# Optimization experiments

Hardware: AMD Instinct MI355X
Metric: run time of the kernel (lower is better)

Reference implementation:

```python
import jax, jax.numpy as jnp
import numpy as np

N = 1_000_000          # number of RoIs
C = 4                  # num_class (foreground classes)
IMG_H, IMG_W = 1080.0, 1920.0
BBOX_MEAN = jnp.array([0.0, 0.0, 0.0, 0.0], jnp.float32)
BBOX_STD = jnp.array([0.1, 0.1, 0.2, 0.2], jnp.float32)
THR_OBJ = 0.2          # threshold_objectness
THR_CLS = 0.1          # thresholds[0]
MIN_W, MIN_H = 6.0, 6.0
MAX_CAND = 300         # nms max_candidate_n
OVERLAP = 0.5          # nms overlap_ratio
TOP_N = 100            # nms top_n


def setup_inputs() -> dict:
    key = jax.random.key(0)
    k1, k2, k3, k4, k5 = jax.random.split(key, 5)
    logits = jax.random.normal(k1, (N, C + 1), jnp.float32) * 2.0
    cls_score_softmax = jax.nn.softmax(logits, axis=-1)          # rows sum to 1, like softmax output
    bbox_pred = jax.random.normal(k2, (N, 4 * (C + 1)), jnp.float32) * 0.5
    x1 = jax.random.uniform(k3, (N,), jnp.float32, 0.0, IMG_W * 0.8)
    y1 = jax.random.uniform(k4, (N,), jnp.float32, 0.0, IMG_H * 0.8)
    wh = jax.random.uniform(k5, (N, 2), jnp.float32, 8.0, 200.0)
    rois = jnp.stack([jnp.zeros((N,), jnp.float32), x1, y1, x1 + wh[:, 0], y1 + wh[:, 1]], axis=1)
    im_info = jnp.array([IMG_H, IMG_W], jnp.float32)
    return {"cls_score_softmax": cls_score_softmax, "bbox_pred": bbox_pred, "rois": rois, "im_info": im_info}


def _pairwise_iou(b):
    # torchvision box_iou convention: area = (x2-x1)*(y2-y1), no +1
    lt = jnp.maximum(b[:, None, :2], b[None, :, :2])
    rb = jnp.minimum(b[:, None, 2:], b[None, :, 2:])
    wh = jnp.clip(rb - lt, 0.0)
    inter = wh[..., 0] * wh[..., 1]
    area = (b[:, 2] - b[:, 0]) * (b[:, 3] - b[:, 1])
    return inter / (area[:, None] + area[None, :] - inter)


def _forward(cls_score_softmax, bbox_pred, rois, im_info):
    h_img, w_img = im_info[0], im_info[1]
    # denormalize deltas and decode against rois (bbox_transform_inv_rcnn)
    deltas = (bbox_pred.reshape(-1, 4) * BBOX_STD + BBOX_MEAN).reshape(-1, C + 1, 4)
    bx = rois[:, 1:]
    w = bx[:, 2] - bx[:, 0] + 1.0
    h = bx[:, 3] - bx[:, 1] + 1.0
    cx = bx[:, 0] + 0.5 * (w - 1.0)
    cy = bx[:, 1] + 0.5 * (h - 1.0)
    pcx = deltas[:, :, 0] * w[:, None] + cx[:, None]
    pcy = deltas[:, :, 1] * h[:, None] + cy[:, None]
    pw = jnp.exp(deltas[:, :, 2]) * w[:, None]
    ph = jnp.exp(deltas[:, :, 3]) * h[:, None]
    pred = jnp.stack([pcx - 0.5 * (pw - 1.0), pcy - 0.5 * (ph - 1.0),
                      pcx + 0.5 * (pw - 1.0), pcy + 0.5 * (ph - 1.0)], axis=-1)  # [N, C+1, 4]
    # refine_out_of_map_bbox: clip to image
    pred = jnp.stack([jnp.clip(pred[..., 0], 0.0, w_img - 1.0),
                      jnp.clip(pred[..., 1], 0.0, h_img - 1.0),
                      jnp.clip(pred[..., 2], 0.0, w_img - 1.0),
                      jnp.clip(pred[..., 3], 0.0, h_img - 1.0)], axis=-1)
    # objectness + class-score filters (masked instead of compacted: jit-friendly)
    mask_obj = (1.0 - cls_score_softmax[:, 0]) >= THR_OBJ
    maxes = jnp.max(cls_score_softmax[:, 1:], axis=1)
    argmaxes = jnp.argmax(cls_score_softmax[:, 1:], axis=1) + 1
    mask_cls = maxes > THR_CLS
    # select the box of the argmax class per row
    box = jnp.take_along_axis(pred, argmaxes[:, None, None], axis=1)[:, 0, :]  # [N, 4]
    bw = box[:, 2] - box[:, 0] + 1.0
    bh = box[:, 3] - box[:, 1] + 1.0
    mask_size = (bw >= MIN_W) | (bh >= MIN_H)  # HEIGHT_OR_WIDTH
    valid = mask_obj & mask_cls & mask_size
    # top-k candidates by max class prob (invalid rows pushed below any real score)
    cand_scores = jnp.where(valid, maxes, -1.0)
    top_vals, top_idx = jax.lax.top_k(cand_scores, MAX_CAND)   # sorted descending
    cand_boxes = box[top_idx]                                   # [M, 4]
    cand_probs = cls_score_softmax[top_idx]                     # [M, C+1]
    cand_valid = top_vals > -0.5
    # greedy NMS over the (score-sorted) candidates
    iou = _pairwise_iou(cand_boxes)
    idx = jnp.arange(MAX_CAND)

    def body(i, keep):
        sup = keep[i] & (iou[i] > OVERLAP) & (idx > i)
        return keep & ~sup

    keep = jax.lax.fori_loop(0, MAX_CAND, body, cand_valid)
    # compact kept rows into the first TOP_N slots (drop-row scatter trick)
    order = jnp.cumsum(keep.astype(jnp.int32)) - 1
    slot = jnp.where(keep & (order < TOP_N), order, TOP_N)
    rows = jnp.concatenate([jnp.zeros((MAX_CAND, 1), cand_boxes.dtype), cand_boxes, cand_probs], axis=1)
    out = jnp.zeros((TOP_N + 1, rows.shape[1]), rows.dtype).at[slot].set(rows)[:TOP_N]
    return out  # [TOP_N, 1 + 4 + (C+1)] = [100, 10], zero-padded past the kept count


def reference(cls_score_softmax, bbox_pred, rois, im_info):
    return _forward(cls_score_softmax, bbox_pred, rois, im_info)
```

## Files before the change

### kernel.cpp

```cpp
#include <hip/hip_runtime.h>
#include <math.h>

#define NBINS 4096
#define CAP   4096
#define MAXC  300
#define MAXCP 320
#define NTASK (MAXC*5)
#define TOPN  100

__device__ __forceinline__ void decode4(float x1, float y1, float x2, float y2,
                                        float4 d4, float Wimg, float Himg,
                                        float& bx1, float& by1, float& bx2, float& by2)
{
    float w  = x2 - x1 + 1.0f;
    float h  = y2 - y1 + 1.0f;
    float cx = x1 + 0.5f*(w - 1.0f);
    float cy = y1 + 0.5f*(h - 1.0f);
    float d0 = d4.x*0.1f, d1 = d4.y*0.1f, d2 = d4.z*0.2f, d3 = d4.w*0.2f;
    float pcx = d0*w + cx;
    float pcy = d1*h + cy;
    float pw  = expf(d2)*w;
    float ph  = expf(d3)*h;
    bx1 = fminf(fmaxf(pcx - 0.5f*(pw-1.0f), 0.0f), Wimg-1.0f);
    by1 = fminf(fmaxf(pcy - 0.5f*(ph-1.0f), 0.0f), Himg-1.0f);
    bx2 = fminf(fmaxf(pcx + 0.5f*(pw-1.0f), 0.0f), Wimg-1.0f);
    by2 = fminf(fmaxf(pcy + 0.5f*(ph-1.0f), 0.0f), Himg-1.0f);
}

__global__ __launch_bounds__(256)
void rcnn_pass1(const float4* __restrict__ cls4, const float4* __restrict__ bbox4,
                const float4* __restrict__ rois4, const float* __restrict__ iminfo,
                float4* __restrict__ scores4,
                unsigned int* __restrict__ hist, unsigned int* __restrict__ counter, int Ng)
{
    if (blockIdx.x == 0) {
        for (int k = threadIdx.x; k < NBINS; k += 256) hist[k] = 0u;
        if (threadIdx.x == 0) *counter = 0u;
    }

    int g = blockIdx.x * blockDim.x + threadIdx.x;
    if (g >= Ng) return;

    float c[20], q[20];
    #pragma unroll
    for (int v = 0; v < 5; v++) {
        float4 cv = cls4[5*g + v];
        c[4*v] = cv.x; c[4*v+1] = cv.y; c[4*v+2] = cv.z; c[4*v+3] = cv.w;
        float4 rv = rois4[5*g + v];
        q[4*v] = rv.x; q[4*v+1] = rv.y; q[4*v+2] = rv.z; q[4*v+3] = rv.w;
    }
    float Himg = iminfo[0], Wimg = iminfo[1];

    float s[4];
    #pragma unroll
    for (int j = 0; j < 4; j++) {
        float p0 = c[5*j], p1 = c[5*j+1], p2 = c[5*j+2], p3 = c[5*j+3], p4 = c[5*j+4];
        float m = p1; int a = 1;
        if (p2 > m) { m = p2; a = 2; }
        if (p3 > m) { m = p3; a = 3; }
        if (p4 > m) { m = p4; a = 4; }
        float sc = -1.0f;
        if (((1.0f - p0) >= 0.2f) && (m > 0.1f)) {
            float4 d4 = bbox4[20*g + 5*j + a];
            float bx1, by1, bx2, by2;
            decode4(q[5*j+1], q[5*j+2], q[5*j+3], q[5*j+4], d4, Wimg, Himg, bx1, by1, bx2, by2);
            float bw = bx2 - bx1 + 1.0f;
            float bh = by2 - by1 + 1.0f;
            if ((bw >= 6.0f) || (bh >= 6.0f)) sc = m;
        }
        s[j] = sc;
    }
    scores4[g] = make_float4(s[0], s[1], s[2], s[3]);
}

__global__ __launch_bounds__(1024)
void rcnn_hist(const float4* __restrict__ scores4, unsigned int* __restrict__ hist, int Ng)
{
    __shared__ unsigned int lh[NBINS];
    const int t = threadIdx.x;
    for (int k = t; k < NBINS; k += 1024) lh[k] = 0u;
    __syncthreads();

    int stride = gridDim.x * 1024;
    for (int g = blockIdx.x * 1024 + t; g < Ng; g += stride) {
        float4 s4 = scores4[g];
        float ss[4] = { s4.x, s4.y, s4.z, s4.w };
        #pragma unroll
        for (int j = 0; j < 4; j++) {
            float s = ss[j];
            if (s > -0.5f) {
                int bin = (int)(s * (float)NBINS);
                bin = bin > NBINS-1 ? NBINS-1 : bin;
                atomicAdd(&lh[bin], 1u);
            }
        }
    }
    __syncthreads();
    for (int k = t; k < NBINS; k += 1024) {
        unsigned int v = lh[k];
        if (v) atomicAdd(&hist[k], v);
    }
}

__global__ __launch_bounds__(64)
void rcnn_pass2(const unsigned int* __restrict__ hist, int* __restrict__ taubin)
{
    const int t = threadIdx.x;
    const uint4* h4 = (const uint4*)hist;
    uint4 v[16];
    #pragma unroll
    for (int j = 0; j < 16; j++) v[j] = h4[t*16 + j];
    unsigned int chunk = 0;
    #pragma unroll
    for (int j = 0; j < 16; j++) chunk += v[j].x + v[j].y + v[j].z + v[j].w;

    unsigned int sfx = chunk;
    #pragma unroll
    for (int d = 1; d < 64; d <<= 1) {
        unsigned int o = __shfl_down(sfx, d, 64);
        if (t + d < 64) sfx += o;
    }
    unsigned int nxt = sfx - chunk;
    bool found = (sfx >= MAXC) && (nxt < MAXC);
    unsigned long long bal = __ballot(found);
    if (found) {
        unsigned int cum = nxt;
        int tau = 64*t;
        #pragma unroll
        for (int k = 15; k >= 0; k--) {
            cum += v[k].w; if (cum >= MAXC) { tau = 64*t + 4*k + 3; goto done; }
            cum += v[k].z; if (cum >= MAXC) { tau = 64*t + 4*k + 2; goto done; }
            cum += v[k].y; if (cum >= MAXC) { tau = 64*t + 4*k + 1; goto done; }
            cum += v[k].x; if (cum >= MAXC) { tau = 64*t + 4*k + 0; goto done; }
        }
        done:
        *taubin = tau;
    }
    if (bal == 0ull && t == 0) *taubin = 0;
}

__global__ __launch_bounds__(256)
void rcnn_pass3(const float4* __restrict__ scores4, const int* __restrict__ taubin,
                float* __restrict__ cscore, int* __restrict__ cidx,
                unsigned int* __restrict__ counter, int Ng)
{
    int g = blockIdx.x * blockDim.x + threadIdx.x;
    if (g >= Ng) return;
    float4 s4 = scores4[g];
    int tau = *taubin;
    float ss[4] = { s4.x, s4.y, s4.z, s4.w };
    #pragma unroll
    for (int j = 0; j < 4; j++) {
        float s = ss[j];
        if (s > -0.5f) {
            int bin = (int)(s * (float)NBINS);
            bin = bin > NBINS-1 ? NBINS-1 : bin;
            if (bin >= tau) {
                unsigned int pos = atomicAdd(counter, 1u);
                if (pos < CAP) { cscore[pos] = s; cidx[pos] = 4*g + j; }
            }
        }
    }
}

__global__ __launch_bounds__(1024)
void rcnn_rank(const float* __restrict__ cls, const float* __restrict__ bbox,
               const float* __restrict__ rois, const float* __restrict__ iminfo,
               const float* __restrict__ cscore, const int* __restrict__ cidx,
               const unsigned int* __restrict__ counter,
               float4* __restrict__ bxg, float* __restrict__ areag,
               float* __restrict__ prg, unsigned long long* __restrict__ maskg)
{
    __shared__ __align__(16) float s_s[CAP];
    __shared__ __align__(16) int   s_id[CAP];
    __shared__ int tid_[MAXC];
    __shared__ unsigned long long maskw[5];
    const int t  = threadIdx.x;
    const int NT = 1024;
    int M = (int)*counter; if (M > CAP) M = CAP;

    for (int i = t; i < M; i += NT)  { s_s[i] = cscore[i]; s_id[i] = cidx[i]; }
    for (int r = t; r < MAXC; r += NT) tid_[r] = -1;
    if (t < 5) maskw[t] = 0ull;
    __syncthreads();

    {
        const float4* sv = (const float4*)s_s;
        const int4*   dv = (const int4*)s_id;
        int M4 = M >> 2;
        for (int i = t; i < M; i += NT) {
            float si = s_s[i]; int di = s_id[i];
            int r = 0;
            for (int jj = 0; jj < M4; jj++) {
                float4 sj = sv[jj]; int4 dj = dv[jj];
                r += (sj.x > si) || (sj.x == si && dj.x < di);
                r += (sj.y > si) || (sj.y == si && dj.y < di);
                r += (sj.z > si) || (sj.z == si && dj.z < di);
                r += (sj.w > si) || (sj.w == si && dj.w < di);
            }
            for (int j = M4 << 2; j < M; j++) {
                float sj = s_s[j]; int dj = s_id[j];
                r += (sj > si) || (sj == si && dj < di);
            }
            if (r < MAXC) tid_[r] = di;
        }
    }
    __syncthreads();

    float Himg = iminfo[0], Wimg = iminfo[1];
    for (int r = t; r < MAXCP; r += NT) {
        int i = (r < MAXC) ? tid_[r] : -1;
        float4 bx = make_float4(0.0f, 0.0f, 0.0f, 0.0f);
        float ar = 0.0f;
        if (i >= 0) {
            float p0 = cls[5*i], p1 = cls[5*i+1], p2 = cls[5*i+2], p3 = cls[5*i+3], p4 = cls[5*i+4];
            prg[5*r+0]=p0; prg[5*r+1]=p1; prg[5*r+2]=p2; prg[5*r+3]=p3; prg[5*r+4]=p4;
            float m = p1; int a = 1;
            if (p2 > m) { m = p2; a = 2; }
            if (p3 > m) { m = p3; a = 3; }
            if (p4 > m) { m = p4; a = 4; }
            float4 d4 = ((const float4*)bbox)[5*i + a];
            float bx1, by1, bx2, by2;
            decode4(rois[5*i+1], rois[5*i+2], rois[5*i+3], rois[5*i+4], d4, Wimg, Himg, bx1, by1, bx2, by2);
            bx = make_float4(bx1, by1, bx2, by2);
            ar = (bx2-bx1)*(by2-by1);
            atomicOr(&maskw[r>>6], 1ull << (r & 63));
        }
        bxg[r] = bx; areag[r] = ar;
    }
    __syncthreads();
    if (t < 5) maskg[t] = maskw[t];
}

__global__ __launch_bounds__(64)
void rcnn_sup(const float4* __restrict__ bxg, const float* __restrict__ areag,
              const unsigned long long* __restrict__ maskg,
              unsigned long long* __restrict__ supg)
{
    __shared__ float4 bxs[MAXCP];
    __shared__ float  ars[MAXCP];
    const int t = threadIdx.x;
    for (int r = t; r < MAXCP; r += 64) { bxs[r] = bxg[r]; ars[r] = areag[r]; }
    __syncthreads();

    int task = blockIdx.x * 64 + t;
    if (task >= NTASK) return;
    int w = task / MAXC;
    int i = task - w * MAXC;
    unsigned long long bits = 0ull;
    int j0 = w << 6;
    if (j0 + 63 > i) {
        float4 bi = bxs[i];
        float areaA = ars[i];
        for (int b = 0; b < 64; b++) {
            int j = j0 + b;
            float4 bj = bxs[j];
            float lx = fmaxf(bi.x, bj.x), ly = fmaxf(bi.y, bj.y);
            float rx = fminf(bi.z, bj.z), ry = fminf(bi.w, bj.w);
            float iw = fmaxf(rx - lx, 0.0f), ih = fmaxf(ry - ly, 0.0f);
            float inter = iw * ih;
            float iou = inter / (areaA + ars[j] - inter);
            bits |= (iou > 0.5f) ? (1ull << b) : 0ull;
        }
        unsigned long long jgt = (i < j0) ? ~0ull
                              : ((i - j0) >= 63 ? 0ull : ~((1ull << (i - j0 + 1)) - 1ull));
        bits &= jgt & maskg[w];
    }
    supg[i*6 + w] = bits;
}

__global__ __launch_bounds__(1024)
void rcnn_scan(const float4* __restrict__ bxg, const float* __restrict__ prg,
               const unsigned long long* __restrict__ maskg,
               const unsigned long long* __restrict__ supg, float* __restrict__ out)
{
    __shared__ __align__(16) unsigned long long sup[MAXC*6];
    __shared__ unsigned long long maskw[5];
    __shared__ float orows[TOPN*10];
    __shared__ int   kept_list[TOPN];
    __shared__ int   s_kept;
    const int t  = threadIdx.x;
    const int NT = 1024;

    {
        const ulonglong2* sg2 = (const ulonglong2*)supg;
        ulonglong2* sl2 = (ulonglong2*)sup;
        for (int k = t; k < (MAXC*6)/2; k += NT) sl2[k] = sg2[k];
    }
    if (t < 5) maskw[t] = maskg[t];
    for (int k = t; k < TOPN*10; k += NT) orows[k] = 0.0f;
    __syncthreads();

    if (t == 0) {
        unsigned long long k0=maskw[0], k1=maskw[1], k2=maskw[2], k3=maskw[3], k4=maskw[4];
        int kept = 0;
        #define SCAN_WORD(W, KW)                                                   \
        if (kept < TOPN) {                                                         \
            unsigned long long donem = 0ull;                                       \
            for (;;) {                                                             \
                unsigned long long rem = (KW) & ~donem;                            \
                if (!rem) break;                                                   \
                int b = __builtin_ctzll(rem);                                      \
                int i = (W << 6) + b;                                              \
                kept_list[kept++] = i;                                             \
                if (kept >= TOPN) break;                                           \
                unsigned long long s0 = sup[i*6+0], s1 = sup[i*6+1],               \
                                   s2 = sup[i*6+2], s3 = sup[i*6+3],               \
                                   s4 = sup[i*6+4];                                \
                k0 &= ~s0; k1 &= ~s1; k2 &= ~s2; k3 &= ~s3; k4 &= ~s4;             \
                donem = (b == 63) ? ~0ull : ((2ull << b) - 1ull);                  \
            }                                                                      \
        }
        SCAN_WORD(0, k0)
        SCAN_WORD(1, k1)
        SCAN_WORD(2, k2)
        SCAN_WORD(3, k3)
        SCAN_WORD(4, k4)
        #undef SCAN_WORD
        s_kept = kept;
    }
    __syncthreads();

    int kept = s_kept;
    if (t < kept) {
        int r = kept_list[t];
        float4 bx = bxg[r];
        float* row = &orows[t*10];
        row[0] = 0.0f;
        row[1] = bx.x; row[2] = bx.y; row[3] = bx.z; row[4] = bx.w;
        row[5] = prg[5*r+0]; row[6] = prg[5*r+1]; row[7] = prg[5*r+2];
        row[8] = prg[5*r+3]; row[9] = prg[5*r+4];
    }
    __syncthreads();
    for (int k = t; k < TOPN*10; k += NT) out[k] = orows[k];
}

extern "C" void kernel_launch(void* const* d_in, const int* in_sizes, int n_in,
                              void* d_out, int out_size, void* d_ws, size_t ws_size,
                              hipStream_t stream)
{
    const float* cls    = (const float*)d_in[0];
    const float* bbox   = (const float*)d_in[1];
    const float* rois   = (const float*)d_in[2];
    const float* iminfo = (const float*)d_in[3];
    int N  = in_sizes[0] / 5;
    int Ng = N / 4;

    char* ws = (char*)d_ws;
    float* scores = (float*)ws;
    size_t off = ((size_t)N * 4 + 255) & ~(size_t)255;
    unsigned int* hist    = (unsigned int*)(ws + off); off += NBINS * 4;
    int*          taubin  = (int*)(ws + off);          off += 256;
    unsigned int* counter = (unsigned int*)(ws + off); off += 256;
    float*        cscore  = (float*)(ws + off);        off += CAP * 4;
    int*          cidx    = (int*)(ws + off);          off += CAP * 4;
    float4*       bxg     = (float4*)(ws + off);       off += MAXCP * 16;
    float*        areag   = (float*)(ws + off);        off += ((MAXCP * 4 + 255) & ~(size_t)255);
    float*        prg     = (float*)(ws + off);        off += ((MAXC * 5 * 4 + 255) & ~(size_t)255);
    unsigned long long* maskg = (unsigned long long*)(ws + off); off += 256;
    unsigned long long* supg  = (unsigned long long*)(ws + off); off += MAXC * 6 * 8;

    int blocksG = (Ng + 255) / 256;
    rcnn_pass1<<<blocksG, 256, 0, stream>>>((const float4*)cls, (const float4*)bbox,
                                            (const float4*)rois, iminfo,
                                            (float4*)scores, hist, counter, Ng);
    rcnn_hist<<<64, 1024, 0, stream>>>((const float4*)scores, hist, Ng);
    rcnn_pass2<<<1, 64, 0, stream>>>(hist, taubin);
    rcnn_pass3<<<blocksG, 256, 0, stream>>>((const float4*)scores, taubin,
                                            cscore, cidx, counter, Ng);
    rcnn_rank<<<1, 1024, 0, stream>>>(cls, bbox, rois, iminfo,
                                      cscore, cidx, counter,
                                      bxg, areag, prg, maskg);
    rcnn_sup<<<(NTASK + 63) / 64, 64, 0, stream>>>(bxg, areag, maskg, supg);
    rcnn_scan<<<1, 1024, 0, stream>>>(bxg, prg, maskg, supg, (float*)d_out);
}
```

Before: 206.5 us.

## Fuse the RCNN post-processing pipeline into a single cooperative grid-synced kernel

Replaces the seven-kernel chain with one cooperative kernel of 256 blocks x 1024 threads, using grid.sync between phases. The phases are scoring plus histogram, global histogram merge, threshold search, candidate compaction, ranking with decode, the IoU suppression bitmask and the greedy scan. The histogram is built in shared memory right in the scoring pass, and scores stay in registers, so the scores buffer is no longer written and re-read. The O(M^2) rank step is spread across all blocks instead of one block. In exchange it adds five grid-wide barriers and depends on the cooperative launch succeeding; if the launch fails, it falls back to the old multi-kernel path.

```diff
diff --git a/kernel.cpp b/kernel.cpp
--- a/kernel.cpp
+++ b/kernel.cpp
@@ -1,5 +1,8 @@
 #include <hip/hip_runtime.h>
+#include <hip/hip_cooperative_groups.h>
 #include <math.h>
+
+namespace cg = cooperative_groups;
 
 #define NBINS 4096
 #define CAP   4096
@@ -7,6 +10,8 @@
 #define MAXCP 320
 #define NTASK (MAXC*5)
 #define TOPN  100
+#define NBLK  256
+#define NTHR  1024
 
 __device__ __forceinline__ void decode4(float x1, float y1, float x2, float y2,
                                         float4 d4, float Wimg, float Himg,
@@ -27,6 +32,287 @@
     by2 = fminf(fmaxf(pcy + 0.5f*(ph-1.0f), 0.0f), Himg-1.0f);
 }
 
+__global__ __launch_bounds__(NTHR)
+void rcnn_mega(const float* __restrict__ cls, const float* __restrict__ bbox,
+               const float* __restrict__ rois, const float* __restrict__ iminfo,
+               char* __restrict__ ws, float* __restrict__ out, int Ng)
+{
+    size_t off = ((size_t)Ng * 16 + 255) & ~(size_t)255;
+    unsigned int* hist    = (unsigned int*)(ws + off); off += NBINS*4;
+    off += 256;
+    unsigned int* counter = (unsigned int*)(ws + off); off += 256;
+    float*  cscore        = (float*)(ws + off);        off += CAP*4;
+    int*    cidx          = (int*)(ws + off);          off += CAP*4;
+    float4* bxg           = (float4*)(ws + off);       off += MAXCP*16;
+    float*  areag         = (float*)(ws + off);        off += ((MAXCP*4 + 255) & ~(size_t)255);
+    float*  prg           = (float*)(ws + off);        off += ((MAXC*5*4 + 255) & ~(size_t)255);
+    unsigned long long* maskg = (unsigned long long*)(ws + off); off += 256;
+    unsigned long long* supg  = (unsigned long long*)(ws + off);
+
+    __shared__ __align__(16) unsigned char u_smem[32768];
+    __shared__ __align__(16) float4 bxs[MAXCP];
+    __shared__ float ars[MAXCP];
+    __shared__ float orows[TOPN*10];
+    __shared__ int   kept_list[TOPN];
+    __shared__ int   s_misc[2];
+
+    cg::grid_group grid = cg::this_grid();
+    const int t   = threadIdx.x;
+    const int bid = blockIdx.x;
+    const int g   = bid * NTHR + t;
+
+    unsigned int* lh = (unsigned int*)u_smem;
+    for (int k = t; k < NBINS; k += NTHR) lh[k] = 0u;
+    if (bid == 0) {
+        for (int k = t; k < NBINS; k += NTHR) hist[k] = 0u;
+        if (t == 0) *counter = 0u;
+        if (t < 5)  maskg[t] = 0ull;
+        for (int r = t; r < MAXCP; r += NTHR) {
+            bxg[r] = make_float4(0.0f, 0.0f, 0.0f, 0.0f);
+            areag[r] = 0.0f;
+        }
+    }
+    __syncthreads();
+
+    float s[4] = { -1.0f, -1.0f, -1.0f, -1.0f };
+    if (g < Ng) {
+        const float4* cls4  = (const float4*)cls;
+        const float4* rois4 = (const float4*)rois;
+        const float4* bbox4 = (const float4*)bbox;
+        float c[20], q[20];
+        #pragma unroll
+        for (int v = 0; v < 5; v++) {
+            float4 cv = cls4[5*g + v];
+            c[4*v] = cv.x; c[4*v+1] = cv.y; c[4*v+2] = cv.z; c[4*v+3] = cv.w;
+            float4 rv = rois4[5*g + v];
+            q[4*v] = rv.x; q[4*v+1] = rv.y; q[4*v+2] = rv.z; q[4*v+3] = rv.w;
+        }
+        float Himg = iminfo[0], Wimg = iminfo[1];
+        #pragma unroll
+        for (int j = 0; j < 4; j++) {
+            float p0 = c[5*j], p1 = c[5*j+1], p2 = c[5*j+2], p3 = c[5*j+3], p4 = c[5*j+4];
+            float m = p1; int a = 1;
+            if (p2 > m) { m = p2; a = 2; }
+            if (p3 > m) { m = p3; a = 3; }
+            if (p4 > m) { m = p4; a = 4; }
+            float sc = -1.0f;
+            if (((1.0f - p0) >= 0.2f) && (m > 0.1f)) {
+                float4 d4 = bbox4[20*g + 5*j + a];
+                float bx1, by1, bx2, by2;
+                decode4(q[5*j+1], q[5*j+2], q[5*j+3], q[5*j+4], d4, Wimg, Himg, bx1, by1, bx2, by2);
+                float bw = bx2 - bx1 + 1.0f;
+                float bh = by2 - by1 + 1.0f;
+                if ((bw >= 6.0f) || (bh >= 6.0f)) sc = m;
+            }
+            s[j] = sc;
+            if (sc > -0.5f) {
+                int bin = (int)(sc * (float)NBINS);
+                bin = bin > NBINS-1 ? NBINS-1 : bin;
+                atomicAdd(&lh[bin], 1u);
+            }
+        }
+    }
+    __threadfence();
+    grid.sync();
+
+    for (int k = t; k < NBINS; k += NTHR) {
+        unsigned int v = lh[k];
+        if (v) atomicAdd(&hist[k], v);
+    }
+    __threadfence();
+    grid.sync();
+
+    if (t < 64) {
+        const uint4* h4 = (const uint4*)hist;
+        uint4 v[16];
+        #pragma unroll
+        for (int j = 0; j < 16; j++) v[j] = h4[t*16 + j];
+        unsigned int chunk = 0;
+        #pragma unroll
+        for (int j = 0; j < 16; j++) chunk += v[j].x + v[j].y + v[j].z + v[j].w;
+        unsigned int sfx = chunk;
+        #pragma unroll
+        for (int d = 1; d < 64; d <<= 1) {
+            unsigned int o = __shfl_down(sfx, d, 64);
+            if (t + d < 64) sfx += o;
+        }
+        unsigned int nxt = sfx - chunk;
+        bool found = (sfx >= MAXC) && (nxt < MAXC);
+        unsigned long long bal = __ballot(found);
+        if (found) {
+            unsigned int cum = nxt;
+            int tauv = 64*t;
+            #pragma unroll
+            for (int k = 15; k >= 0; k--) {
+                cum += v[k].w; if (cum >= MAXC) { tauv = 64*t + 4*k + 3; goto dtau; }
+                cum += v[k].z; if (cum >= MAXC) { tauv = 64*t + 4*k + 2; goto dtau; }
+                cum += v[k].y; if (cum >= MAXC) { tauv = 64*t + 4*k + 1; goto dtau; }
+                cum += v[k].x; if (cum >= MAXC) { tauv = 64*t + 4*k + 0; goto dtau; }
+            }
+            dtau:
+            s_misc[0] = tauv;
+        }
+        if (bal == 0ull && t == 0) s_misc[0] = 0;
+    }
+    __syncthreads();
+    {
+        int tau = s_misc[0];
+        if (g < Ng) {
+            #pragma unroll
+            for (int j = 0; j < 4; j++) {
+                float sc = s[j];
+                if (sc > -0.5f) {
+                    int bin = (int)(sc * (float)NBINS);
+                    bin = bin > NBINS-1 ? NBINS-1 : bin;
+                    if (bin >= tau) {
+                        unsigned int pos = atomicAdd(counter, 1u);
+                        if (pos < CAP) { cscore[pos] = sc; cidx[pos] = 4*g + j; }
+                    }
+                }
+            }
+        }
+    }
+    __threadfence();
+    grid.sync();
+
+    {
+        float* s_s  = (float*)u_smem;
+        int*   s_id = (int*)(u_smem + CAP*4);
+        int M = (int)*counter; if (M > CAP) M = CAP;
+        for (int i = t; i < M; i += NTHR) { s_s[i] = cscore[i]; s_id[i] = cidx[i]; }
+        __syncthreads();
+
+        int C = (M + NBLK - 1) / NBLK;
+        float Himg = iminfo[0], Wimg = iminfo[1];
+        const float4* sv = (const float4*)s_s;
+        const int4*   dv = (const int4*)s_id;
+        int M4 = M >> 2;
+        for (int ii = t; ii < C; ii += NTHR) {
+            int i = bid * C + ii;
+            if (i < M) {
+                float si = s_s[i]; int di = s_id[i];
+                int r = 0;
+                for (int jj = 0; jj < M4; jj++) {
+                    float4 sj = sv[jj]; int4 dj = dv[jj];
+                    r += (sj.x > si) || (sj.x == si && dj.x < di);
+                    r += (sj.y > si) || (sj.y == si && dj.y < di);
+                    r += (sj.z > si) || (sj.z == si && dj.z < di);
+                    r += (sj.w > si) || (sj.w == si && dj.w < di);
+                }
+                for (int j = M4 << 2; j < M; j++) {
+                    float sj = s_s[j]; int dj = s_id[j];
+                    r += (sj > si) || (sj == si && dj < di);
+                }
+                if (r < MAXC) {
+                    int idx = di;
+                    float p0 = cls[5*idx], p1 = cls[5*idx+1], p2 = cls[5*idx+2],
+                          p3 = cls[5*idx+3], p4 = cls[5*idx+4];
+                    prg[5*r+0]=p0; prg[5*r+1]=p1; prg[5*r+2]=p2; prg[5*r+3]=p3; prg[5*r+4]=p4;
+                    float m = p1; int a = 1;
+                    if (p2 > m) { m = p2; a = 2; }
+                    if (p3 > m) { m = p3; a = 3; }
+                    if (p4 > m) { m = p4; a = 4; }
+                    float4 d4 = ((const float4*)bbox)[5*idx + a];
+                    float bx1, by1, bx2, by2;
+                    decode4(rois[5*idx+1], rois[5*idx+2], rois[5*idx+3], rois[5*idx+4],
+                            d4, Wimg, Himg, bx1, by1, bx2, by2);
+                    bxg[r] = make_float4(bx1, by1, bx2, by2);
+                    areag[r] = (bx2-bx1)*(by2-by1);
+                    atomicOr(&maskg[r>>6], 1ull << (r & 63));
+                }
+            }
+        }
+    }
+    __threadfence();
+    grid.sync();
+
+    {
+        for (int r = t; r < MAXCP; r += NTHR) { bxs[r] = bxg[r]; ars[r] = areag[r]; }
+        __syncthreads();
+        if (t < 6) {
+            int task = bid * 6 + t;
+            if (task < NTASK) {
+                int w = task / MAXC;
+                int i = task - w * MAXC;
+                unsigned long long bits = 0ull;
+                int j0 = w << 6;
+                if (j0 + 63 > i) {
+                    float4 bi = bxs[i];
+                    float areaA = ars[i];
+                    for (int b = 0; b < 64; b++) {
+                        int j = j0 + b;
+                        float4 bj = bxs[j];
+                        float lx = fmaxf(bi.x, bj.x), ly = fmaxf(bi.y, bj.y);
+                        float rx = fminf(bi.z, bj.z), ry = fminf(bi.w, bj.w);
+                        float iw = fmaxf(rx - lx, 0.0f), ih = fmaxf(ry - ly, 0.0f);
+                        float inter = iw * ih;
+                        float iou = inter / (areaA + ars[j] - inter);
+                        bits |= (iou > 0.5f) ? (1ull << b) : 0ull;
+                    }
+                    unsigned long long jgt = (i < j0) ? ~0ull
+                                          : ((i - j0) >= 63 ? 0ull : ~((1ull << (i - j0 + 1)) - 1ull));
+                    bits &= jgt & maskg[w];
+                }
+                supg[i*6 + w] = bits;
+            }
+        }
+    }
+    __threadfence();
+    grid.sync();
+
+    if (bid == 0) {
+        unsigned long long* sup = (unsigned long long*)u_smem;
+        const ulonglong2* sg2 = (const ulonglong2*)supg;
+        ulonglong2* sl2 = (ulonglong2*)sup;
+        for (int k = t; k < (MAXC*6)/2; k += NTHR) sl2[k] = sg2[k];
+        for (int k = t; k < TOPN*10; k += NTHR) orows[k] = 0.0f;
+        __syncthreads();
+
+        if (t == 0) {
+            unsigned long long k0=maskg[0], k1=maskg[1], k2=maskg[2], k3=maskg[3], k4=maskg[4];
+            int kept = 0;
+            #define SCAN_WORD(W, KW)                                                   \
+            if (kept < TOPN) {                                                         \
+                unsigned long long donem = 0ull;                                       \
+                for (;;) {                                                             \
+                    unsigned long long rem = (KW) & ~donem;                            \
+                    if (!rem) break;                                                   \
+                    int b = __builtin_ctzll(rem);                                      \
+                    int i = (W << 6) + b;                                              \
+                    kept_list[kept++] = i;                                             \
+                    if (kept >= TOPN) break;                                           \
+                    unsigned long long s0 = sup[i*6+0], s1 = sup[i*6+1],               \
+                                       s2 = sup[i*6+2], s3 = sup[i*6+3],               \
+                                       s4 = sup[i*6+4];                                \
+                    k0 &= ~s0; k1 &= ~s1; k2 &= ~s2; k3 &= ~s3; k4 &= ~s4;             \
+                    donem = (b == 63) ? ~0ull : ((2ull << b) - 1ull);                  \
+                }                                                                      \
+            }
+            SCAN_WORD(0, k0)
+            SCAN_WORD(1, k1)
+            SCAN_WORD(2, k2)
+            SCAN_WORD(3, k3)
+            SCAN_WORD(4, k4)
+            #undef SCAN_WORD
+            s_misc[1] = kept;
+        }
+        __syncthreads();
+
+        int kept = s_misc[1];
+        if (t < kept) {
+            int r = kept_list[t];
+            float4 bx = bxg[r];
+            float* row = &orows[t*10];
+            row[0] = 0.0f;
+            row[1] = bx.x; row[2] = bx.y; row[3] = bx.z; row[4] = bx.w;
+            row[5] = prg[5*r+0]; row[6] = prg[5*r+1]; row[7] = prg[5*r+2];
+            row[8] = prg[5*r+3]; row[9] = prg[5*r+4];
+        }
+        __syncthreads();
+        for (int k = t; k < TOPN*10; k += NTHR) out[k] = orows[k];
+    }
+}
+
 __global__ __launch_bounds__(256)
 void rcnn_pass1(const float4* __restrict__ cls4, const float4* __restrict__ bbox4,
                 const float4* __restrict__ rois4, const float* __restrict__ iminfo,
@@ -37,10 +323,8 @@
         for (int k = threadIdx.x; k < NBINS; k += 256) hist[k] = 0u;
         if (threadIdx.x == 0) *counter = 0u;
     }
-
     int g = blockIdx.x * blockDim.x + threadIdx.x;
     if (g >= Ng) return;
-
     float c[20], q[20];
     #pragma unroll
     for (int v = 0; v < 5; v++) {
@@ -50,7 +334,6 @@
         q[4*v] = rv.x; q[4*v+1] = rv.y; q[4*v+2] = rv.z; q[4*v+3] = rv.w;
     }
     float Himg = iminfo[0], Wimg = iminfo[1];
-
     float s[4];
     #pragma unroll
     for (int j = 0; j < 4; j++) {
@@ -80,7 +363,6 @@
     const int t = threadIdx.x;
     for (int k = t; k < NBINS; k += 1024) lh[k] = 0u;
     __syncthreads();
-
     int stride = gridDim.x * 1024;
     for (int g = blockIdx.x * 1024 + t; g < Ng; g += stride) {
         float4 s4 = scores4[g];
@@ -113,7 +395,6 @@
     unsigned int chunk = 0;
     #pragma unroll
     for (int j = 0; j < 16; j++) chunk += v[j].x + v[j].y + v[j].z + v[j].w;
-
     unsigned int sfx = chunk;
     #pragma unroll
     for (int d = 1; d < 64; d <<= 1) {
@@ -178,12 +459,10 @@
     const int t  = threadIdx.x;
     const int NT = 1024;
     int M = (int)*counter; if (M > CAP) M = CAP;
-
     for (int i = t; i < M; i += NT)  { s_s[i] = cscore[i]; s_id[i] = cidx[i]; }
     for (int r = t; r < MAXC; r += NT) tid_[r] = -1;
     if (t < 5) maskw[t] = 0ull;
     __syncthreads();
-
     {
         const float4* sv = (const float4*)s_s;
         const int4*   dv = (const int4*)s_id;
@@ -206,7 +485,6 @@
         }
     }
     __syncthreads();
-
     float Himg = iminfo[0], Wimg = iminfo[1];
     for (int r = t; r < MAXCP; r += NT) {
         int i = (r < MAXC) ? tid_[r] : -1;
@@ -242,7 +520,6 @@
     const int t = threadIdx.x;
     for (int r = t; r < MAXCP; r += 64) { bxs[r] = bxg[r]; ars[r] = areag[r]; }
     __syncthreads();
-
     int task = blockIdx.x * 64 + t;
     if (task >= NTASK) return;
     int w = task / MAXC;
@@ -281,7 +558,6 @@
     __shared__ int   s_kept;
     const int t  = threadIdx.x;
     const int NT = 1024;
-
     {
         const ulonglong2* sg2 = (const ulonglong2*)supg;
         ulonglong2* sl2 = (ulonglong2*)sup;
@@ -290,7 +566,6 @@
     if (t < 5) maskw[t] = maskg[t];
     for (int k = t; k < TOPN*10; k += NT) orows[k] = 0.0f;
     __syncthreads();
-
     if (t == 0) {
         unsigned long long k0=maskw[0], k1=maskw[1], k2=maskw[2], k3=maskw[3], k4=maskw[4];
         int kept = 0;
@@ -320,7 +595,6 @@
         s_kept = kept;
     }
     __syncthreads();
-
     int kept = s_kept;
     if (t < kept) {
         int r = kept_list[t];
@@ -346,7 +620,16 @@
     int N  = in_sizes[0] / 5;
     int Ng = N / 4;
 
-    char* ws = (char*)d_ws;
+    char*  ws   = (char*)d_ws;
+    float* outp = (float*)d_out;
+
+    void* args[] = { (void*)&cls, (void*)&bbox, (void*)&rois, (void*)&iminfo,
+                     (void*)&ws, (void*)&outp, (void*)&Ng };
+    hipError_t e = hipLaunchCooperativeKernel((void*)rcnn_mega, dim3(NBLK), dim3(NTHR),
+                                              args, 0, stream);
+    if (e == hipSuccess) return;
+    (void)hipGetLastError();
+
     float* scores = (float*)ws;
     size_t off = ((size_t)N * 4 + 255) & ~(size_t)255;
     unsigned int* hist    = (unsigned int*)(ws + off); off += NBINS * 4;
@@ -372,5 +655,5 @@
                                       cscore, cidx, counter,
                                       bxg, areag, prg, maskg);
     rcnn_sup<<<(NTASK + 63) / 64, 64, 0, stream>>>(bxg, areag, maskg, supg);
-    rcnn_scan<<<1, 1024, 0, stream>>>(bxg, prg, maskg, supg, (float*)d_out);
-}
+    rcnn_scan<<<1, 1024, 0, stream>>>(bxg, prg, maskg, supg, outp);
+}
```

New measurement: 742.2 us. 3.59x slower.

## Fuse threshold search into select pass and prefetch next NMS suppression row

Applied to the files above, without the earlier changes.

The single-block kernel that scanned the histogram for the threshold bin is removed. Every block of the candidate-select kernel now recomputes the threshold from the 4096-bin histogram with its first wavefront and shares it through shared memory, which saves one launch and its serialization gap but adds redundant histogram reads in every block. The serial greedy NMS scan is also rewritten as a next-set-bit walk that loads the next candidate's suppression row before the current one is applied, hiding shared-memory latency on the single-thread critical path.

```diff
diff --git a/kernel.cpp b/kernel.cpp
--- a/kernel.cpp
+++ b/kernel.cpp
@@ -27,6 +27,21 @@
     by2 = fminf(fmaxf(pcy + 0.5f*(ph-1.0f), 0.0f), Himg-1.0f);
 }
 
+__device__ __forceinline__ int nb5(unsigned long long k0, unsigned long long k1,
+                                   unsigned long long k2, unsigned long long k3,
+                                   unsigned long long k4, int from)
+{
+    if (from >= MAXC) return MAXC;
+    int w = from >> 6;
+    unsigned long long first = ~0ull << (from & 63);
+    if (w <= 0) { unsigned long long m = k0 & (w == 0 ? first : ~0ull); if (m) return       __builtin_ctzll(m); }
+    if (w <= 1) { unsigned long long m = k1 & (w == 1 ? first : ~0ull); if (m) return  64 + __builtin_ctzll(m); }
+    if (w <= 2) { unsigned long long m = k2 & (w == 2 ? first : ~0ull); if (m) return 128 + __builtin_ctzll(m); }
+    if (w <= 3) { unsigned long long m = k3 & (w == 3 ? first : ~0ull); if (m) return 192 + __builtin_ctzll(m); }
+    {           unsigned long long m = k4 & (w == 4 ? first : ~0ull); if (m) return 256 + __builtin_ctzll(m); }
+    return MAXC;
+}
+
 __global__ __launch_bounds__(256)
 void rcnn_pass1(const float4* __restrict__ cls4, const float4* __restrict__ bbox4,
                 const float4* __restrict__ rois4, const float* __restrict__ iminfo,
@@ -37,10 +52,8 @@
         for (int k = threadIdx.x; k < NBINS; k += 256) hist[k] = 0u;
         if (threadIdx.x == 0) *counter = 0u;
     }
-
     int g = blockIdx.x * blockDim.x + threadIdx.x;
     if (g >= Ng) return;
-
     float c[20], q[20];
     #pragma unroll
     for (int v = 0; v < 5; v++) {
@@ -50,7 +63,6 @@
         q[4*v] = rv.x; q[4*v+1] = rv.y; q[4*v+2] = rv.z; q[4*v+3] = rv.w;
     }
     float Himg = iminfo[0], Wimg = iminfo[1];
-
     float s[4];
     #pragma unroll
     for (int j = 0; j < 4; j++) {
@@ -80,7 +92,6 @@
     const int t = threadIdx.x;
     for (int k = t; k < NBINS; k += 1024) lh[k] = 0u;
     __syncthreads();
-
     int stride = gridDim.x * 1024;
     for (int g = blockIdx.x * 1024 + t; g < Ng; g += stride) {
         float4 s4 = scores4[g];
@@ -102,52 +113,51 @@
     }
 }
 
-__global__ __launch_bounds__(64)
-void rcnn_pass2(const unsigned int* __restrict__ hist, int* __restrict__ taubin)
-{
+__global__ __launch_bounds__(256)
+void rcnn_pass3t(const float4* __restrict__ scores4, const unsigned int* __restrict__ hist,
+                 float* __restrict__ cscore, int* __restrict__ cidx,
+                 unsigned int* __restrict__ counter, int Ng)
+{
+    __shared__ int s_tau;
     const int t = threadIdx.x;
-    const uint4* h4 = (const uint4*)hist;
-    uint4 v[16];
-    #pragma unroll
-    for (int j = 0; j < 16; j++) v[j] = h4[t*16 + j];
-    unsigned int chunk = 0;
-    #pragma unroll
-    for (int j = 0; j < 16; j++) chunk += v[j].x + v[j].y + v[j].z + v[j].w;
-
-    unsigned int sfx = chunk;
-    #pragma unroll
-    for (int d = 1; d < 64; d <<= 1) {
-        unsigned int o = __shfl_down(sfx, d, 64);
-        if (t + d < 64) sfx += o;
-    }
-    unsigned int nxt = sfx - chunk;
-    bool found = (sfx >= MAXC) && (nxt < MAXC);
-    unsigned long long bal = __ballot(found);
-    if (found) {
-        unsigned int cum = nxt;
-        int tau = 64*t;
+    if (t < 64) {
+        const uint4* h4 = (const uint4*)hist;
+        uint4 v[16];
         #pragma unroll
-        for (int k = 15; k >= 0; k--) {
-            cum += v[k].w; if (cum >= MAXC) { tau = 64*t + 4*k + 3; goto done; }
-            cum += v[k].z; if (cum >= MAXC) { tau = 64*t + 4*k + 2; goto done; }
-            cum += v[k].y; if (cum >= MAXC) { tau = 64*t + 4*k + 1; goto done; }
-            cum += v[k].x; if (cum >= MAXC) { tau = 64*t + 4*k + 0; goto done; }
-        }
-        done:
-        *taubin = tau;
-    }
-    if (bal == 0ull && t == 0) *taubin = 0;
-}
-
-__global__ __launch_bounds__(256)
-void rcnn_pass3(const float4* __restrict__ scores4, const int* __restrict__ taubin,
-                float* __restrict__ cscore, int* __restrict__ cidx,
-                unsigned int* __restrict__ counter, int Ng)
-{
-    int g = blockIdx.x * blockDim.x + threadIdx.x;
+        for (int j = 0; j < 16; j++) v[j] = h4[t*16 + j];
+        unsigned int chunk = 0;
+        #pragma unroll
+        for (int j = 0; j < 16; j++) chunk += v[j].x + v[j].y + v[j].z + v[j].w;
+        unsigned int sfx = chunk;
+        #pragma unroll
+        for (int d = 1; d < 64; d <<= 1) {
+            unsigned int o = __shfl_down(sfx, d, 64);
+            if (t + d < 64) sfx += o;
+        }
+        unsigned int nxt = sfx - chunk;
+        bool found = (sfx >= MAXC) && (nxt < MAXC);
+        unsigned long long bal = __ballot(found);
+        if (found) {
+            unsigned int cum = nxt;
+            int tauv = 64*t;
+            #pragma unroll
+            for (int k = 15; k >= 0; k--) {
+                cum += v[k].w; if (cum >= MAXC) { tauv = 64*t + 4*k + 3; goto dtau; }
+                cum += v[k].z; if (cum >= MAXC) { tauv = 64*t + 4*k + 2; goto dtau; }
+                cum += v[k].y; if (cum >= MAXC) { tauv = 64*t + 4*k + 1; goto dtau; }
+                cum += v[k].x; if (cum >= MAXC) { tauv = 64*t + 4*k + 0; goto dtau; }
+            }
+            dtau:
+            s_tau = tauv;
+        }
+        if (bal == 0ull && t == 0) s_tau = 0;
+    }
+    __syncthreads();
+    int tau = s_tau;
+
+    int g = blockIdx.x * blockDim.x + t;
     if (g >= Ng) return;
     float4 s4 = scores4[g];
-    int tau = *taubin;
     float ss[4] = { s4.x, s4.y, s4.z, s4.w };
     #pragma unroll
     for (int j = 0; j < 4; j++) {
@@ -178,7 +188,6 @@
     const int t  = threadIdx.x;
     const int NT = 1024;
     int M = (int)*counter; if (M > CAP) M = CAP;
-
     for (int i = t; i < M; i += NT)  { s_s[i] = cscore[i]; s_id[i] = cidx[i]; }
     for (int r = t; r < MAXC; r += NT) tid_[r] = -1;
     if (t < 5) maskw[t] = 0ull;
@@ -242,7 +251,6 @@
     const int t = threadIdx.x;
     for (int r = t; r < MAXCP; r += 64) { bxs[r] = bxg[r]; ars[r] = areag[r]; }
     __syncthreads();
-
     int task = blockIdx.x * 64 + t;
     if (task >= NTASK) return;
     int w = task / MAXC;
@@ -275,7 +283,6 @@
                const unsigned long long* __restrict__ supg, float* __restrict__ out)
 {
     __shared__ __align__(16) unsigned long long sup[MAXC*6];
-    __shared__ unsigned long long maskw[5];
     __shared__ float orows[TOPN*10];
     __shared__ int   kept_list[TOPN];
     __shared__ int   s_kept;
@@ -287,36 +294,35 @@
         ulonglong2* sl2 = (ulonglong2*)sup;
         for (int k = t; k < (MAXC*6)/2; k += NT) sl2[k] = sg2[k];
     }
-    if (t < 5) maskw[t] = maskg[t];
     for (int k = t; k < TOPN*10; k += NT) orows[k] = 0.0f;
     __syncthreads();
 
     if (t == 0) {
-        unsigned long long k0=maskw[0], k1=maskw[1], k2=maskw[2], k3=maskw[3], k4=maskw[4];
+        unsigned long long k0=maskg[0], k1=maskg[1], k2=maskg[2], k3=maskg[3], k4=maskg[4];
         int kept = 0;
-        #define SCAN_WORD(W, KW)                                                   \
-        if (kept < TOPN) {                                                         \
-            unsigned long long donem = 0ull;                                       \
-            for (;;) {                                                             \
-                unsigned long long rem = (KW) & ~donem;                            \
-                if (!rem) break;                                                   \
-                int b = __builtin_ctzll(rem);                                      \
-                int i = (W << 6) + b;                                              \
-                kept_list[kept++] = i;                                             \
-                if (kept >= TOPN) break;                                           \
-                unsigned long long s0 = sup[i*6+0], s1 = sup[i*6+1],               \
-                                   s2 = sup[i*6+2], s3 = sup[i*6+3],               \
-                                   s4 = sup[i*6+4];                                \
-                k0 &= ~s0; k1 &= ~s1; k2 &= ~s2; k3 &= ~s3; k4 &= ~s4;             \
-                donem = (b == 63) ? ~0ull : ((2ull << b) - 1ull);                  \
-            }                                                                      \
-        }
-        SCAN_WORD(0, k0)
-        SCAN_WORD(1, k1)
-        SCAN_WORD(2, k2)
-        SCAN_WORD(3, k3)
-        SCAN_WORD(4, k4)
-        #undef SCAN_WORD
+        int specp = -1;
+        unsigned long long h0=0ull,h1=0ull,h2=0ull,h3=0ull,h4=0ull;
+        int cur = nb5(k0,k1,k2,k3,k4, 0);
+        while (cur < MAXC && kept < TOPN) {
+            kept_list[kept++] = cur;
+            if (kept >= TOPN) break;
+            unsigned long long r0,r1,r2,r3,r4;
+            if (cur == specp) { r0=h0; r1=h1; r2=h2; r3=h3; r4=h4; }
+            else {
+                const ulonglong2* rp = (const ulonglong2*)&sup[cur*6];
+                ulonglong2 ra = rp[0], rb = rp[1];
+                r0=ra.x; r1=ra.y; r2=rb.x; r3=rb.y; r4=sup[cur*6+4];
+            }
+            int spec = nb5(k0,k1,k2,k3,k4, cur+1);
+            if (spec < MAXC) {
+                const ulonglong2* sp = (const ulonglong2*)&sup[spec*6];
+                ulonglong2 sa = sp[0], sb = sp[1];
+                h0=sa.x; h1=sa.y; h2=sb.x; h3=sb.y; h4=sup[spec*6+4];
+                specp = spec;
+            } else specp = -1;
+            k0 &= ~r0; k1 &= ~r1; k2 &= ~r2; k3 &= ~r3; k4 &= ~r4;
+            cur = nb5(k0,k1,k2,k3,k4, cur+1);
+        }
         s_kept = kept;
     }
     __syncthreads();
@@ -350,7 +356,7 @@
     float* scores = (float*)ws;
     size_t off = ((size_t)N * 4 + 255) & ~(size_t)255;
     unsigned int* hist    = (unsigned int*)(ws + off); off += NBINS * 4;
-    int*          taubin  = (int*)(ws + off);          off += 256;
+    int*          taubin  = (int*)(ws + off);          off += 256;  (void)taubin;
     unsigned int* counter = (unsigned int*)(ws + off); off += 256;
     float*        cscore  = (float*)(ws + off);        off += CAP * 4;
     int*          cidx    = (int*)(ws + off);          off += CAP * 4;
@@ -365,9 +371,8 @@
                                             (const float4*)rois, iminfo,
                                             (float4*)scores, hist, counter, Ng);
     rcnn_hist<<<64, 1024, 0, stream>>>((const float4*)scores, hist, Ng);
-    rcnn_pass2<<<1, 64, 0, stream>>>(hist, taubin);
-    rcnn_pass3<<<blocksG, 256, 0, stream>>>((const float4*)scores, taubin,
-                                            cscore, cidx, counter, Ng);
+    rcnn_pass3t<<<blocksG, 256, 0, stream>>>((const float4*)scores, hist,
+                                             cscore, cidx, counter, Ng);
     rcnn_rank<<<1, 1024, 0, stream>>>(cls, bbox, rois, iminfo,
                                       cscore, cidx, counter,
                                       bxg, areag, prg, maskg);
```

New measurement: 220.4 us. +6.8%, slower.
